# Performance work log

Measured on AMD Instinct MI355X. Metric: run time of the kernel, lower is better.

## Reference

```python
import jax, jax.numpy as jnp
import numpy as np
from jax.scipy.special import logsumexp

N = 512   # hidden states (obs_number)
M = 256   # emission symbols == sequence length (raw_number)
B = 128   # batch


def setup_inputs() -> dict:
    key = jax.random.key(0)
    k1, k2, k3, k4 = jax.random.split(key, 4)
    return {
        "obs": jax.random.randint(k1, (B, M), 0, M),
        "unnormalized_state_priors": jax.random.normal(k2, (N,), dtype=jnp.float32),
        "unnormalized_transition_matrix": jax.random.normal(k3, (N, N), dtype=jnp.float32),
        "unnormalized_emission_matrix": jax.random.normal(k4, (N, M), dtype=jnp.float32),
    }


def reference(obs, unnormalized_state_priors, unnormalized_transition_matrix,
              unnormalized_emission_matrix):
    # Normalized matrices are computed ONCE (the torch code redundantly
    # recomputes them every timestep; the math is identical).
    log_priors = jax.nn.log_softmax(unnormalized_state_priors)                 # [N]
    log_T = jax.nn.log_softmax(unnormalized_transition_matrix, axis=0)         # [N,N], T[i,k]=P(i|k)
    log_E = jax.nn.log_softmax(unnormalized_emission_matrix, axis=1)           # [N,M]

    # Emission log-probs per timestep: em[b,t,i] = log_E[i, obs[b,t]] -> [B,M,N]
    em = jnp.moveaxis(log_E[:, obs], 0, -1)

    alpha0 = em[:, 0, :] + log_priors                                          # [B,N]

    def step(a_prev, e_t):
        # log-domain matmul: a[b,i] = logsumexp_k( log_T[i,k] + a_prev[b,k] )
        a = e_t + logsumexp(log_T[None, :, :] + a_prev[:, None, :], axis=-1)   # [B,N]
        return a, logsumexp(a, axis=-1)                                        # carry, per-t log-sum

    em_tm = jnp.swapaxes(em, 0, 1)                                             # time-major [M,B,N]
    _, ls_rest = jax.lax.scan(step, alpha0, em_tm[1:])                         # [M-1,B]

    ls0 = logsumexp(alpha0, axis=-1)                                           # [B]
    log_sums = jnp.concatenate([ls0[:, None], ls_rest.T], axis=1)              # [B,M]
    return log_sums
```

## Files before the change

### kernel.cpp

```cpp
#include <hip/hip_runtime.h>
#include <hip/hip_bf16.h>
#include <math.h>

#define NN 512
#define MM 256
#define BB 128

typedef float        f32x4 __attribute__((ext_vector_type(4)));
typedef unsigned int u32;
typedef u32          u32x2 __attribute__((ext_vector_type(2)));
typedef unsigned long long u64;
typedef int          i32x8 __attribute__((ext_vector_type(8)));

#define LOG16F 2.772588722239781f
#define SCL1   0x7F

__device__ __forceinline__ float wave_max(float v) {
#pragma unroll
    for (int o = 32; o > 0; o >>= 1) v = fmaxf(v, __shfl_xor(v, o));
    return v;
}
__device__ __forceinline__ float wave_sum(float v) {
#pragma unroll
    for (int o = 32; o > 0; o >>= 1) v += __shfl_xor(v, o);
    return v;
}


__global__ void k_col_lse(const float* __restrict__ T, float* __restrict__ c) {
    int k = blockIdx.x * 64 + threadIdx.x;
    float m = -INFINITY, s = 0.f;
    for (int i = 0; i < NN; ++i) {
        float x = T[i * NN + k];
        if (x > m) { s = s * __expf(m - x) + 1.f; m = x; }
        else       { s += __expf(x - m); }
    }
    c[k] = m + __logf(s);
}

__global__ void k_rowM(const float* __restrict__ T, const float* __restrict__ c,
                       float* __restrict__ M) {
    int i = blockIdx.x, j = threadIdx.x;
    float mx = -INFINITY;
#pragma unroll
    for (int d = 0; d < 8; ++d) {
        int k = j * 8 + d;
        mx = fmaxf(mx, T[i * NN + k] - c[k]);
    }
    mx = wave_max(mx);
    if (j == 0) M[i] = mx - __logf(64.f);
}

__global__ void k_cm(const float* __restrict__ M, float* __restrict__ CM) {
    __shared__ float red[8];
    int i = threadIdx.x;
    float wm = wave_max(M[i]);
    if ((i & 63) == 0) red[i >> 6] = wm;
    __syncthreads();
    if (i == 0) {
        float m = red[0];
#pragma unroll
        for (int j = 1; j < 8; ++j) m = fmaxf(m, red[j]);
        CM[0] = m;
    }
}

__global__ void k_priors(const float* __restrict__ pr, const float* __restrict__ M,
                         const float* __restrict__ CM, float* __restrict__ lp2) {
    __shared__ float red[8];
    int i = threadIdx.x;
    float x = pr[i];
    float wm = wave_max(x);
    if ((i & 63) == 0) red[i >> 6] = wm;
    __syncthreads();
    float m = red[0];
#pragma unroll
    for (int j = 1; j < 8; ++j) m = fmaxf(m, red[j]);
    float e = __expf(x - m);
    float ws = wave_sum(e);
    __syncthreads();
    if ((i & 63) == 0) red[i >> 6] = ws;
    __syncthreads();
    float S = red[0];
#pragma unroll
    for (int j = 1; j < 8; ++j) S += red[j];
    float lp = x - (m + __logf(S));
    lp2[i] = __expf(lp - M[i] + CM[0] + LOG16F);
}

__global__ void k_packA(const float* __restrict__ T, const float* __restrict__ c,
                        const float* __restrict__ M, u32* __restrict__ PA) {
    int blk = blockIdx.x, l = threadIdx.x;
    int tile = blk >> 2, kc = blk & 3;
    int row = tile * 16 + (l & 15);
    int kb  = kc * 128 + (l >> 4) * 32;
    float Mi = M[row];
    i32x8 dd;
#pragma unroll
    for (int q = 0; q < 8; ++q) {
        float p0 = __expf(T[row * NN + kb + 4*q + 0] - c[kb + 4*q + 0] - Mi);
        float p1 = __expf(T[row * NN + kb + 4*q + 1] - c[kb + 4*q + 1] - Mi);
        float p2 = __expf(T[row * NN + kb + 4*q + 2] - c[kb + 4*q + 2] - Mi);
        float p3 = __expf(T[row * NN + kb + 4*q + 3] - c[kb + 4*q + 3] - Mi);
        int d = 0;
        d = __builtin_amdgcn_cvt_pk_fp8_f32(p0, p1, d, false);
        d = __builtin_amdgcn_cvt_pk_fp8_f32(p2, p3, d, true);
        dd[q] = d;
    }
    *(i32x8*)(PA + ((size_t)blk * 64 + l) * 8) = dd;
}

__global__ void k_rowEX(const float* __restrict__ E, const float* __restrict__ M,
                        const float* __restrict__ CM, float* __restrict__ EX) {
    int i = blockIdx.x, j = threadIdx.x;
    float v[4];
    float mx = -INFINITY;
#pragma unroll
    for (int d = 0; d < 4; ++d) {
        v[d] = E[i * MM + j * 4 + d];
        mx = fmaxf(mx, v[d]);
    }
    mx = wave_max(mx);
    float s = 0.f;
#pragma unroll
    for (int d = 0; d < 4; ++d) s += __expf(v[d] - mx);
    s = wave_sum(s);
    float lse = mx + __logf(s);
    float add = M[i] - CM[0] - LOG16F - lse;
#pragma unroll
    for (int d = 0; d < 4; ++d)
        EX[(size_t)(j * 4 + d) * NN + i] = __expf(v[d] + add);
}

__global__ __launch_bounds__(512, 2) void k_scan(
        const int* __restrict__ obs, const float* __restrict__ lp2,
        const float* __restrict__ CM, const u32* __restrict__ PAu,
        const float* __restrict__ EX, float* __restrict__ out) {
    int b = blockIdx.x, tid = threadIdx.x;
    int w = tid >> 6, l = tid & 63;
    int h32 = (l >> 4) * 32;
    int r4 = (l >> 4) * 4;
    __shared__ unsigned char us8[NN] __attribute__((aligned(64)));
    __shared__ float rB[8] __attribute__((aligned(16)));
    __shared__ int obs_s[MM];
    if (tid < MM) obs_s[tid] = obs[b * MM + tid];

    i32x8 pa[16];
#pragma unroll
    for (int ti = 0; ti < 4; ++ti)
#pragma unroll
        for (int kc = 0; kc < 4; ++kc)
            pa[ti * 4 + kc] = *(const i32x8*)(PAu
                + ((size_t)(((w * 4 + ti) * 4 + kc) * 64) + l) * 8);
#pragma unroll
    for (int q = 0; q < 16; ++q) asm volatile("" : "+a"(pa[q]));

    float C_M = CM[0];
    int ubase[4];
#pragma unroll
    for (int ti = 0; ti < 4; ++ti) ubase[ti] = (w * 4 + ti) * 16 + r4;
    __syncthreads();

    int o0 = obs_s[0];
    f32x4 e4[4];
    float loc = 0.f;
#pragma unroll
    for (int ti = 0; ti < 4; ++ti) {
        f32x4 ex  = *(const f32x4*)(EX  + (size_t)o0 * NN + (w * 4 + ti) * 16 + r4);
        f32x4 lpv = *(const f32x4*)(lp2 + (w * 4 + ti) * 16 + r4);
#pragma unroll
        for (int r = 0; r < 4; ++r) {
            float e = ex[r] * lpv[r];
            e4[ti][r] = e; loc += e;
        }
    }
    loc += __shfl_xor(loc, 16);
    loc += __shfl_xor(loc, 32);
    if (l == 0) rB[w] = loc;
    __syncthreads();
    f32x4 sv0 = *(const f32x4*)rB;
    f32x4 sv1 = *(const f32x4*)(rB + 4);
    float S = (sv0[0] + sv0[1]) + (sv0[2] + sv0[3])
            + (sv1[0] + sv1[1]) + (sv1[2] + sv1[3]);
    S = fmaxf(S, 1e-35f);
    float sc = __builtin_amdgcn_rcpf(S) * 16.f;
    if ((l & 15) == 0) {
#pragma unroll
        for (int ti = 0; ti < 4; ++ti) {
            int d = 0;
            d = __builtin_amdgcn_cvt_pk_fp8_f32(e4[ti][0] * sc, e4[ti][1] * sc, d, false);
            d = __builtin_amdgcn_cvt_pk_fp8_f32(e4[ti][2] * sc, e4[ti][3] * sc, d, true);
            *(u32*)&us8[ubase[ti]] = (u32)d;
        }
    }
    __syncthreads();
    float lS = __logf(S);
    if (tid == 0) out[(size_t)b * MM + 0] = lS;
    float K = C_M + lS;

    f32x4 exn[4];
    {
        int on = obs_s[1];
#pragma unroll
        for (int ti = 0; ti < 4; ++ti)
            exn[ti] = *(const f32x4*)(EX + (size_t)on * NN + (w * 4 + ti) * 16 + r4);
    }

#pragma unroll 1
    for (int t = 1; t < MM; ++t) {
        const unsigned char* ub = us8;
        f32x4 a0 = {0.f,0.f,0.f,0.f}, a1 = {0.f,0.f,0.f,0.f};
        f32x4 a2 = {0.f,0.f,0.f,0.f}, a3 = {0.f,0.f,0.f,0.f};
        __builtin_amdgcn_s_setprio(1);
#pragma unroll
        for (int kc = 0; kc < 4; ++kc) {
            i32x8 bb = *(const i32x8*)(ub + kc * 128 + h32);
            a0 = __builtin_amdgcn_mfma_scale_f32_16x16x128_f8f6f4(
                     pa[0 * 4 + kc], bb, a0, 0, 0, 0, SCL1, 0, SCL1);
            a1 = __builtin_amdgcn_mfma_scale_f32_16x16x128_f8f6f4(
                     pa[1 * 4 + kc], bb, a1, 0, 0, 0, SCL1, 0, SCL1);
            a2 = __builtin_amdgcn_mfma_scale_f32_16x16x128_f8f6f4(
                     pa[2 * 4 + kc], bb, a2, 0, 0, 0, SCL1, 0, SCL1);
            a3 = __builtin_amdgcn_mfma_scale_f32_16x16x128_f8f6f4(
                     pa[3 * 4 + kc], bb, a3, 0, 0, 0, SCL1, 0, SCL1);
        }
        __builtin_amdgcn_s_setprio(0);
        f32x4 sacc[4] = { a0, a1, a2, a3 };

        loc = 0.f;
#pragma unroll
        for (int ti = 0; ti < 4; ++ti)
#pragma unroll
            for (int r = 0; r < 4; ++r) {
                float e = exn[ti][r] * sacc[ti][r];
                e4[ti][r] = e; loc += e;
            }

        int on = obs_s[(t + 1 < MM) ? t + 1 : t];
#pragma unroll
        for (int ti = 0; ti < 4; ++ti)
            exn[ti] = *(const f32x4*)(EX + (size_t)on * NN + (w * 4 + ti) * 16 + r4);

        loc += __shfl_xor(loc, 16);
        loc += __shfl_xor(loc, 32);
        if (l == 0) rB[w] = loc;
        __syncthreads();
        sv0 = *(const f32x4*)rB;
        sv1 = *(const f32x4*)(rB + 4);
        S = (sv0[0] + sv0[1]) + (sv0[2] + sv0[3])
          + (sv1[0] + sv1[1]) + (sv1[2] + sv1[3]);
        S = fmaxf(S, 1e-35f);
        sc = __builtin_amdgcn_rcpf(S) * 16.f;
        if ((l & 15) == 0) {
#pragma unroll
            for (int ti = 0; ti < 4; ++ti) {
                int d = 0;
                d = __builtin_amdgcn_cvt_pk_fp8_f32(e4[ti][0] * sc, e4[ti][1] * sc, d, false);
                d = __builtin_amdgcn_cvt_pk_fp8_f32(e4[ti][2] * sc, e4[ti][3] * sc, d, true);
                *(u32*)&us8[ubase[ti]] = (u32)d;
            }
        }
        __syncthreads();
        float lSn = __logf(S);
        if (tid == 0) out[(size_t)b * MM + t] = K + lSn;
        K += C_M + lSn;
    }
}

extern "C" void kernel_launch(void* const* d_in, const int* in_sizes, int n_in,
                              void* d_out, int out_size, void* d_ws, size_t ws_size,
                              hipStream_t stream) {
    const int*   obs = (const int*)d_in[0];
    const float* pri = (const float*)d_in[1];
    const float* T   = (const float*)d_in[2];
    const float* E   = (const float*)d_in[3];
    float* out = (float*)d_out;
    char* ws = (char*)d_ws;

    float* c   = (float*)(ws + 0);
    float* lp2 = (float*)(ws + 2048);
    float* M   = (float*)(ws + 4096);
    float* CM  = (float*)(ws + 6144);
    u32*   PA  = (u32*)(ws + 8192);
    float* EX  = (float*)(ws + 8192 + 256 * 1024);

    k_col_lse<<<8,   64, 0, stream>>>(T, c);
    k_rowM   <<<512, 64, 0, stream>>>(T, c, M);
    k_cm     <<<1,  512, 0, stream>>>(M, CM);
    k_priors <<<1,  512, 0, stream>>>(pri, M, CM, lp2);
    k_packA  <<<128, 64, 0, stream>>>(T, c, M, PA);
    k_rowEX  <<<512, 64, 0, stream>>>(E, M, CM, EX);
    k_scan   <<<BB, 512, 0, stream>>>(obs, lp2, CM, PA, EX, out);
}
```

Before: 390.7 us.

## Fuse preprocessing kernels, parallelize column LSE, split MFMA accumulator chains

Column log-sum-exp now runs one wave per column, with a wave-level reduction, instead of a serial 512-iteration loop over only 8 blocks. The CM, priors, packA and rowEX kernels are merged into one k_prep launch, and every block recomputes the global max of M itself, which removes three launches and their serialization. In the scan loop the K=512 reduction is split into two independent accumulator chains that are summed at the end, shortening the dependent MFMA chain. The cost is redundant max reductions in each block and extra accumulator registers.

```diff
diff --git a/kernel.cpp b/kernel.cpp
--- a/kernel.cpp
+++ b/kernel.cpp
@@ -28,14 +28,17 @@
 
 
 __global__ void k_col_lse(const float* __restrict__ T, float* __restrict__ c) {
-    int k = blockIdx.x * 64 + threadIdx.x;
+    int k = blockIdx.x, j = threadIdx.x;
     float m = -INFINITY, s = 0.f;
-    for (int i = 0; i < NN; ++i) {
-        float x = T[i * NN + k];
+#pragma unroll
+    for (int q = 0; q < 8; ++q) {
+        float x = T[(q * 64 + j) * NN + k];
         if (x > m) { s = s * __expf(m - x) + 1.f; m = x; }
         else       { s += __expf(x - m); }
     }
-    c[k] = m + __logf(s);
+    float mw = wave_max(m);
+    float sw = wave_sum(s * __expf(m - mw));
+    if (j == 0) c[k] = mw + __logf(sw);
 }
 
 __global__ void k_rowM(const float* __restrict__ T, const float* __restrict__ c,
@@ -51,90 +54,83 @@
     if (j == 0) M[i] = mx - __logf(64.f);
 }
 
-__global__ void k_cm(const float* __restrict__ M, float* __restrict__ CM) {
-    __shared__ float red[8];
-    int i = threadIdx.x;
-    float wm = wave_max(M[i]);
-    if ((i & 63) == 0) red[i >> 6] = wm;
-    __syncthreads();
-    if (i == 0) {
-        float m = red[0];
-#pragma unroll
-        for (int j = 1; j < 8; ++j) m = fmaxf(m, red[j]);
-        CM[0] = m;
-    }
-}
-
-__global__ void k_priors(const float* __restrict__ pr, const float* __restrict__ M,
-                         const float* __restrict__ CM, float* __restrict__ lp2) {
-    __shared__ float red[8];
-    int i = threadIdx.x;
-    float x = pr[i];
-    float wm = wave_max(x);
-    if ((i & 63) == 0) red[i >> 6] = wm;
-    __syncthreads();
-    float m = red[0];
-#pragma unroll
-    for (int j = 1; j < 8; ++j) m = fmaxf(m, red[j]);
-    float e = __expf(x - m);
-    float ws = wave_sum(e);
-    __syncthreads();
-    if ((i & 63) == 0) red[i >> 6] = ws;
-    __syncthreads();
-    float S = red[0];
-#pragma unroll
-    for (int j = 1; j < 8; ++j) S += red[j];
-    float lp = x - (m + __logf(S));
-    lp2[i] = __expf(lp - M[i] + CM[0] + LOG16F);
-}
-
-__global__ void k_packA(const float* __restrict__ T, const float* __restrict__ c,
-                        const float* __restrict__ M, u32* __restrict__ PA) {
+__global__ void k_prep(const float* __restrict__ T, const float* __restrict__ c,
+                       const float* __restrict__ M, const float* __restrict__ pr,
+                       const float* __restrict__ E,
+                       float* __restrict__ lp2, u32* __restrict__ PA,
+                       float* __restrict__ EX) {
     int blk = blockIdx.x, l = threadIdx.x;
-    int tile = blk >> 2, kc = blk & 3;
-    int row = tile * 16 + (l & 15);
-    int kb  = kc * 128 + (l >> 4) * 32;
-    float Mi = M[row];
-    i32x8 dd;
-#pragma unroll
-    for (int q = 0; q < 8; ++q) {
-        float p0 = __expf(T[row * NN + kb + 4*q + 0] - c[kb + 4*q + 0] - Mi);
-        float p1 = __expf(T[row * NN + kb + 4*q + 1] - c[kb + 4*q + 1] - Mi);
-        float p2 = __expf(T[row * NN + kb + 4*q + 2] - c[kb + 4*q + 2] - Mi);
-        float p3 = __expf(T[row * NN + kb + 4*q + 3] - c[kb + 4*q + 3] - Mi);
-        int d = 0;
-        d = __builtin_amdgcn_cvt_pk_fp8_f32(p0, p1, d, false);
-        d = __builtin_amdgcn_cvt_pk_fp8_f32(p2, p3, d, true);
-        dd[q] = d;
-    }
-    *(i32x8*)(PA + ((size_t)blk * 64 + l) * 8) = dd;
-}
-
-__global__ void k_rowEX(const float* __restrict__ E, const float* __restrict__ M,
-                        const float* __restrict__ CM, float* __restrict__ EX) {
-    int i = blockIdx.x, j = threadIdx.x;
-    float v[4];
-    float mx = -INFINITY;
-#pragma unroll
-    for (int d = 0; d < 4; ++d) {
-        v[d] = E[i * MM + j * 4 + d];
-        mx = fmaxf(mx, v[d]);
-    }
-    mx = wave_max(mx);
-    float s = 0.f;
-#pragma unroll
-    for (int d = 0; d < 4; ++d) s += __expf(v[d] - mx);
-    s = wave_sum(s);
-    float lse = mx + __logf(s);
-    float add = M[i] - CM[0] - LOG16F - lse;
-#pragma unroll
-    for (int d = 0; d < 4; ++d)
-        EX[(size_t)(j * 4 + d) * NN + i] = __expf(v[d] + add);
+    if (blk < 512) {
+        float mm = -INFINITY;
+#pragma unroll
+        for (int q = 0; q < 8; ++q) mm = fmaxf(mm, M[q * 64 + l]);
+        float CMv = wave_max(mm);
+        int i = blk;
+        float v[4];
+        float mx = -INFINITY;
+#pragma unroll
+        for (int d = 0; d < 4; ++d) {
+            v[d] = E[i * MM + l * 4 + d];
+            mx = fmaxf(mx, v[d]);
+        }
+        mx = wave_max(mx);
+        float s = 0.f;
+#pragma unroll
+        for (int d = 0; d < 4; ++d) s += __expf(v[d] - mx);
+        s = wave_sum(s);
+        float lse = mx + __logf(s);
+        float add = M[i] - CMv - LOG16F - lse;
+#pragma unroll
+        for (int d = 0; d < 4; ++d)
+            EX[(size_t)(l * 4 + d) * NN + i] = __expf(v[d] + add);
+    } else if (blk < 640) {
+        int bb = blk - 512;
+        int tile = bb >> 2, kc = bb & 3;
+        int row = tile * 16 + (l & 15);
+        int kb  = kc * 128 + (l >> 4) * 32;
+        float Mi = M[row];
+        i32x8 dd;
+#pragma unroll
+        for (int q = 0; q < 8; ++q) {
+            float p0 = __expf(T[row * NN + kb + 4*q + 0] - c[kb + 4*q + 0] - Mi);
+            float p1 = __expf(T[row * NN + kb + 4*q + 1] - c[kb + 4*q + 1] - Mi);
+            float p2 = __expf(T[row * NN + kb + 4*q + 2] - c[kb + 4*q + 2] - Mi);
+            float p3 = __expf(T[row * NN + kb + 4*q + 3] - c[kb + 4*q + 3] - Mi);
+            int d = 0;
+            d = __builtin_amdgcn_cvt_pk_fp8_f32(p0, p1, d, false);
+            d = __builtin_amdgcn_cvt_pk_fp8_f32(p2, p3, d, true);
+            dd[q] = d;
+        }
+        *(i32x8*)(PA + ((size_t)bb * 64 + l) * 8) = dd;
+    } else {
+        float mm = -INFINITY;
+#pragma unroll
+        for (int q = 0; q < 8; ++q) mm = fmaxf(mm, M[q * 64 + l]);
+        float CMv = wave_max(mm);
+        float x[8];
+        float mx = -INFINITY;
+#pragma unroll
+        for (int q = 0; q < 8; ++q) {
+            x[q] = pr[q * 64 + l];
+            mx = fmaxf(mx, x[q]);
+        }
+        mx = wave_max(mx);
+        float s = 0.f;
+#pragma unroll
+        for (int q = 0; q < 8; ++q) s += __expf(x[q] - mx);
+        s = wave_sum(s);
+        float lse = mx + __logf(s);
+#pragma unroll
+        for (int q = 0; q < 8; ++q) {
+            int i = q * 64 + l;
+            lp2[i] = __expf(x[q] - lse - M[i] + CMv + LOG16F);
+        }
+    }
 }
 
 __global__ __launch_bounds__(512, 2) void k_scan(
         const int* __restrict__ obs, const float* __restrict__ lp2,
-        const float* __restrict__ CM, const u32* __restrict__ PAu,
+        const float* __restrict__ Mrow, const u32* __restrict__ PAu,
         const float* __restrict__ EX, float* __restrict__ out) {
     int b = blockIdx.x, tid = threadIdx.x;
     int w = tid >> 6, l = tid & 63;
@@ -145,6 +141,11 @@
     __shared__ int obs_s[MM];
     if (tid < MM) obs_s[tid] = obs[b * MM + tid];
 
+    float mm = -INFINITY;
+#pragma unroll
+    for (int q = 0; q < 8; ++q) mm = fmaxf(mm, Mrow[q * 64 + l]);
+    float C_M = wave_max(mm);
+
     i32x8 pa[16];
 #pragma unroll
     for (int ti = 0; ti < 4; ++ti)
@@ -155,7 +156,6 @@
 #pragma unroll
     for (int q = 0; q < 16; ++q) asm volatile("" : "+a"(pa[q]));
 
-    float C_M = CM[0];
     int ubase[4];
 #pragma unroll
     for (int ti = 0; ti < 4; ++ti) ubase[ti] = (w * 4 + ti) * 16 + r4;
@@ -211,21 +211,32 @@
         const unsigned char* ub = us8;
         f32x4 a0 = {0.f,0.f,0.f,0.f}, a1 = {0.f,0.f,0.f,0.f};
         f32x4 a2 = {0.f,0.f,0.f,0.f}, a3 = {0.f,0.f,0.f,0.f};
+        f32x4 b0 = {0.f,0.f,0.f,0.f}, b1 = {0.f,0.f,0.f,0.f};
+        f32x4 b2 = {0.f,0.f,0.f,0.f}, b3 = {0.f,0.f,0.f,0.f};
         __builtin_amdgcn_s_setprio(1);
 #pragma unroll
-        for (int kc = 0; kc < 4; ++kc) {
-            i32x8 bb = *(const i32x8*)(ub + kc * 128 + h32);
+        for (int kc = 0; kc < 2; ++kc) {
+            i32x8 bbA = *(const i32x8*)(ub + kc * 128 + h32);
+            i32x8 bbB = *(const i32x8*)(ub + (kc + 2) * 128 + h32);
             a0 = __builtin_amdgcn_mfma_scale_f32_16x16x128_f8f6f4(
-                     pa[0 * 4 + kc], bb, a0, 0, 0, 0, SCL1, 0, SCL1);
+                     pa[0 * 4 + kc], bbA, a0, 0, 0, 0, SCL1, 0, SCL1);
             a1 = __builtin_amdgcn_mfma_scale_f32_16x16x128_f8f6f4(
-                     pa[1 * 4 + kc], bb, a1, 0, 0, 0, SCL1, 0, SCL1);
+                     pa[1 * 4 + kc], bbA, a1, 0, 0, 0, SCL1, 0, SCL1);
             a2 = __builtin_amdgcn_mfma_scale_f32_16x16x128_f8f6f4(
-                     pa[2 * 4 + kc], bb, a2, 0, 0, 0, SCL1, 0, SCL1);
+                     pa[2 * 4 + kc], bbA, a2, 0, 0, 0, SCL1, 0, SCL1);
             a3 = __builtin_amdgcn_mfma_scale_f32_16x16x128_f8f6f4(
-                     pa[3 * 4 + kc], bb, a3, 0, 0, 0, SCL1, 0, SCL1);
+                     pa[3 * 4 + kc], bbA, a3, 0, 0, 0, SCL1, 0, SCL1);
+            b0 = __builtin_amdgcn_mfma_scale_f32_16x16x128_f8f6f4(
+                     pa[0 * 4 + kc + 2], bbB, b0, 0, 0, 0, SCL1, 0, SCL1);
+            b1 = __builtin_amdgcn_mfma_scale_f32_16x16x128_f8f6f4(
+                     pa[1 * 4 + kc + 2], bbB, b1, 0, 0, 0, SCL1, 0, SCL1);
+            b2 = __builtin_amdgcn_mfma_scale_f32_16x16x128_f8f6f4(
+                     pa[2 * 4 + kc + 2], bbB, b2, 0, 0, 0, SCL1, 0, SCL1);
+            b3 = __builtin_amdgcn_mfma_scale_f32_16x16x128_f8f6f4(
+                     pa[3 * 4 + kc + 2], bbB, b3, 0, 0, 0, SCL1, 0, SCL1);
         }
         __builtin_amdgcn_s_setprio(0);
-        f32x4 sacc[4] = { a0, a1, a2, a3 };
+        f32x4 sacc[4] = { a0 + b0, a1 + b1, a2 + b2, a3 + b3 };
 
         loc = 0.f;
 #pragma unroll
@@ -280,15 +291,11 @@
     float* c   = (float*)(ws + 0);
     float* lp2 = (float*)(ws + 2048);
     float* M   = (float*)(ws + 4096);
-    float* CM  = (float*)(ws + 6144);
     u32*   PA  = (u32*)(ws + 8192);
     float* EX  = (float*)(ws + 8192 + 256 * 1024);
 
-    k_col_lse<<<8,   64, 0, stream>>>(T, c);
+    k_col_lse<<<512, 64, 0, stream>>>(T, c);
     k_rowM   <<<512, 64, 0, stream>>>(T, c, M);
-    k_cm     <<<1,  512, 0, stream>>>(M, CM);
-    k_priors <<<1,  512, 0, stream>>>(pri, M, CM, lp2);
-    k_packA  <<<128, 64, 0, stream>>>(T, c, M, PA);
-    k_rowEX  <<<512, 64, 0, stream>>>(E, M, CM, EX);
-    k_scan   <<<BB, 512, 0, stream>>>(obs, lp2, CM, PA, EX, out);
-}
+    k_prep   <<<641, 64, 0, stream>>>(T, c, M, pri, E, lp2, PA, EX);
+    k_scan   <<<BB, 512, 0, stream>>>(obs, lp2, M, PA, EX, out);
+}
```

Measured after the change: 327.1 us. 16.3% less time.
